# Optimization experiments

Measured on AMD Instinct MI355X. Metric: run time of the kernel, lower is better.

Reference implementation:

```python
import jax, jax.numpy as jnp
import numpy as np

EPS = 1e-12  # torch F.normalize eps

def _normalize(x, axis=-1):
    n = jnp.linalg.norm(x, axis=axis, keepdims=True)
    return x / jnp.maximum(n, EPS)

def setup_inputs() -> dict:
    key = jax.random.key(0)
    ks = jax.random.split(key, 6)
    B, D_in, T, Dc, K = 16, 1024, 4096, 8, 1024
    return {
        "z": jax.random.normal(ks[0], (B, D_in, T), jnp.float32),
        "in_w": jax.random.normal(ks[1], (Dc, D_in), jnp.float32) * 0.02,
        "in_b": jax.random.normal(ks[2], (Dc,), jnp.float32) * 0.02,
        "out_w": jax.random.normal(ks[3], (D_in, Dc), jnp.float32) * 0.02,
        "out_b": jax.random.normal(ks[4], (D_in,), jnp.float32) * 0.02,
        "codebook": jax.random.normal(ks[5], (K, Dc), jnp.float32),
    }

def reference(z, in_w, in_b, out_w, out_b, codebook):
    sg = jax.lax.stop_gradient
    # in_proj: kernel-size-1 conv == per-timestep linear. z: [B, D_in, T] -> z_e: [B, Dc, T]
    z_e = jnp.einsum('od,bdt->bot', in_w, z) + in_b[None, :, None]
    zt = jnp.swapaxes(z_e, 1, 2)  # [B, T, Dc]
    B, T, Dc = zt.shape
    # decode_latents: cosine-normalized squared-distance argmin over codebook
    en = _normalize(zt)                      # [B, T, Dc]
    cn = _normalize(codebook)                # [K, Dc]
    dist = (jnp.sum(en * en, -1, keepdims=True)
            - 2.0 * jnp.einsum('btd,kd->btk', en, cn)
            + jnp.sum(cn * cn, -1)[None, None, :])  # [B, T, K]
    indices = jnp.argmax(-dist, axis=-1)     # [B, T] int
    zq_td = codebook[indices]                # [B, T, Dc] (gather from unnormalized codebook)
    # losses (mean over channel+time dims per batch element)
    commitment_loss = jnp.mean((zt - sg(zq_td)) ** 2, axis=(1, 2))
    codebook_loss = jnp.mean((zq_td - sg(zt)) ** 2, axis=(1, 2))
    # rotation trick: R = I - 2 r r^T + 2 q e^T, applied fused (never materialize BxTxDxD)
    e_norm = _normalize(sg(zt))
    q_norm = _normalize(sg(zq_td))
    r = _normalize(e_norm + q_norm)
    scaling = (jnp.linalg.norm(sg(zq_td), axis=-1)
               / jnp.clip(jnp.linalg.norm(sg(zt), axis=-1), 1e-8))[..., None]
    Rz = zt - 2.0 * r * jnp.sum(r * zt, -1, keepdims=True) \
            + 2.0 * q_norm * jnp.sum(e_norm * zt, -1, keepdims=True)
    zq_rot = scaling * Rz                    # [B, T, Dc]
    zq = jnp.swapaxes(zq_rot, 1, 2)          # [B, Dc, T]
    # out_proj
    z_q_out = jnp.einsum('od,bdt->bot', out_w, zq) + out_b[None, :, None]  # [B, D_in, T]
    return (z_q_out, commitment_loss, codebook_loss, indices.astype(jnp.int32), z_e)
```

## Files before the change

kernel.cpp:

```cpp
#include <hip/hip_runtime.h>
#include <math.h>

#define NB   16
#define DIN  1024
#define TT   4096
#define DC   8
#define NK   1024
#define TA   128
#define NTA  (TT/TA)
#define NPG  16
#define KCP  (NK/NPG)

#define OFF_CL  ((size_t)NB*DIN*TT)
#define OFF_CB  (OFF_CL + NB)
#define OFF_IDX (OFF_CB + NB)
#define OFF_ZE  (OFF_IDX + (size_t)NB*TT)

__global__ __launch_bounds__(512, 4) void vq_mega(const float* __restrict__ z,
    const float* __restrict__ in_w, const float* __restrict__ in_b,
    const float* __restrict__ out_w, const float* __restrict__ out_b,
    const float* __restrict__ cbk, float* __restrict__ dout,
    float* __restrict__ lpart)
{
  __shared__ float regA[DIN*DC];
  __shared__ float regB[8*TA*DC];
  __shared__ float ze_s[DC*TA];
  float2* cand = (float2*)regB;
  float*  cn2  = regB + 4096;
  float*  obs  = regB + 5120;
  float*  zq_s = regB + 6144;
  float*  lred = regB + 7168;

  const int tid = threadIdx.x;
  const int tb = blockIdx.x, b = blockIdx.y;
  const int t0 = tb*TA;

  for (int i = tid; i < DIN*DC; i += 512) {
    const int d = i >> 3, o = i & 7;
    regA[i] = in_w[o*DIN + d];
  }
  __syncthreads();
  {
    const int sub = tid >> 6, l = tid & 63;
    const int dbase = sub*128;
    const float* zp = z + ((size_t)b*DIN + dbase)*TT + t0 + 2*l;
    float ax[DC], ay[DC];
    #pragma unroll
    for (int o = 0; o < DC; ++o) { ax[o] = 0.f; ay[o] = 0.f; }
    #pragma unroll 8
    for (int d = 0; d < 128; ++d) {
      const float2 v = *(const float2*)&zp[(size_t)d*TT];
      const float4 w0 = *(const float4*)&regA[(dbase+d)*DC];
      const float4 w1 = *(const float4*)&regA[(dbase+d)*DC+4];
      ax[0] = fmaf(v.x, w0.x, ax[0]);  ay[0] = fmaf(v.y, w0.x, ay[0]);
      ax[1] = fmaf(v.x, w0.y, ax[1]);  ay[1] = fmaf(v.y, w0.y, ay[1]);
      ax[2] = fmaf(v.x, w0.z, ax[2]);  ay[2] = fmaf(v.y, w0.z, ay[2]);
      ax[3] = fmaf(v.x, w0.w, ax[3]);  ay[3] = fmaf(v.y, w0.w, ay[3]);
      ax[4] = fmaf(v.x, w1.x, ax[4]);  ay[4] = fmaf(v.y, w1.x, ay[4]);
      ax[5] = fmaf(v.x, w1.y, ax[5]);  ay[5] = fmaf(v.y, w1.y, ay[5]);
      ax[6] = fmaf(v.x, w1.z, ax[6]);  ay[6] = fmaf(v.y, w1.z, ay[6]);
      ax[7] = fmaf(v.x, w1.w, ax[7]);  ay[7] = fmaf(v.y, w1.w, ay[7]);
    }
    float* pa = &regB[((size_t)sub*TA + 2*l)*DC];
    *(float4*)&pa[0]    = make_float4(ax[0], ax[1], ax[2], ax[3]);
    *(float4*)&pa[4]    = make_float4(ax[4], ax[5], ax[6], ax[7]);
    *(float4*)&pa[DC]   = make_float4(ay[0], ay[1], ay[2], ay[3]);
    *(float4*)&pa[DC+4] = make_float4(ay[4], ay[5], ay[6], ay[7]);
  }
  __syncthreads();
  {
    const int t = tid & 127, oq = tid >> 7;
    const int o0 = 2*oq;
    float2 p = *(const float2*)&regB[(0*TA + t)*DC + o0];
    float s0 = p.x, s1 = p.y;
    #pragma unroll
    for (int c = 1; c < 8; ++c) {
      p = *(const float2*)&regB[(c*TA + t)*DC + o0];
      s0 += p.x; s1 += p.y;
    }
    const float v0 = s0 + in_b[o0];
    const float v1 = s1 + in_b[o0+1];
    ze_s[o0*TA + t]     = v0;
    ze_s[(o0+1)*TA + t] = v1;
    dout[OFF_ZE + ((size_t)b*DC + o0)*TT + t0 + t]     = v0;
    dout[OFF_ZE + ((size_t)b*DC + o0+1)*TT + t0 + t]   = v1;
  }
  __syncthreads();

  for (int k = tid; k < NK; k += 512) {
    float c[DC];
    const float4 c0 = *(const float4*)&cbk[k*DC];
    const float4 c1 = *(const float4*)&cbk[k*DC+4];
    c[0]=c0.x; c[1]=c0.y; c[2]=c0.z; c[3]=c0.w;
    c[4]=c1.x; c[5]=c1.y; c[6]=c1.z; c[7]=c1.w;
    float ss = 0.f;
    #pragma unroll
    for (int i = 0; i < DC; ++i) ss = fmaf(c[i], c[i], ss);
    const float den = fmaxf(sqrtf(ss), 1e-12f);
    float s2 = 0.f;
    #pragma unroll
    for (int i = 0; i < DC; ++i) { const float v = c[i]/den; regA[k*DC+i] = v; s2 = fmaf(v, v, s2); }
    cn2[k] = s2;
  }
  __syncthreads();

  {
    const int pg = tid >> 5, l = tid & 31;
    const int k0 = pg*KCP;
    float en[4][DC], en2v[4];
    #pragma unroll
    for (int m = 0; m < 4; ++m) {
      const int t = l + 32*m;
      float e[DC];
      #pragma unroll
      for (int o = 0; o < DC; ++o) e[o] = ze_s[o*TA + t];
      float se = 0.f;
      #pragma unroll
      for (int i = 0; i < DC; ++i) se = fmaf(e[i], e[i], se);
      const float dene = fmaxf(sqrtf(se), 1e-12f);
      float s2 = 0.f;
      #pragma unroll
      for (int i = 0; i < DC; ++i) { en[m][i] = e[i]/dene; s2 = fmaf(en[m][i], en[m][i], s2); }
      en2v[m] = s2;
    }
    float bd[4]; int bk[4];
    #pragma unroll
    for (int m = 0; m < 4; ++m) { bd[m] = 3.4e38f; bk[m] = k0; }
    #pragma unroll 2
    for (int k = 0; k < KCP; ++k) {
      const float4 a0 = *(const float4*)&regA[(k0+k)*DC];
      const float4 a1 = *(const float4*)&regA[(k0+k)*DC+4];
      const float c2 = cn2[k0+k];
      #pragma unroll
      for (int m = 0; m < 4; ++m) {
        float dacc = en[m][0]*a0.x;
        dacc = fmaf(en[m][1], a0.y, dacc);
        dacc = fmaf(en[m][2], a0.z, dacc);
        dacc = fmaf(en[m][3], a0.w, dacc);
        dacc = fmaf(en[m][4], a1.x, dacc);
        dacc = fmaf(en[m][5], a1.y, dacc);
        dacc = fmaf(en[m][6], a1.z, dacc);
        dacc = fmaf(en[m][7], a1.w, dacc);
        const float dist = (en2v[m] - 2.0f*dacc) + c2;
        if (dist < bd[m]) { bd[m] = dist; bk[m] = k0 + k; }
      }
    }
    #pragma unroll
    for (int m = 0; m < 4; ++m)
      cand[pg*TA + l + 32*m] = make_float2(bd[m], __int_as_float(bk[m]));
  }
  __syncthreads();

  if (tid < TA) {
    float bdm = cand[tid].x;
    int bkm = __float_as_int(cand[tid].y);
    #pragma unroll
    for (int p = 1; p < NPG; ++p) {
      const float2 c = cand[p*TA + tid];
      if (c.x < bdm) { bdm = c.x; bkm = __float_as_int(c.y); }
    }
    dout[OFF_IDX + (size_t)b*TT + t0 + tid] = (float)bkm;

    float e[DC], en_[DC];
    #pragma unroll
    for (int o = 0; o < DC; ++o) e[o] = ze_s[o*TA + tid];
    float se = 0.f;
    #pragma unroll
    for (int i = 0; i < DC; ++i) se = fmaf(e[i], e[i], se);
    const float ne = sqrtf(se);
    const float dene = fmaxf(ne, 1e-12f);
    #pragma unroll
    for (int i = 0; i < DC; ++i) en_[i] = e[i]/dene;

    float q[DC];
    {
      const float4 q0 = *(const float4*)&cbk[bkm*DC];
      const float4 q1 = *(const float4*)&cbk[bkm*DC+4];
      q[0]=q0.x; q[1]=q0.y; q[2]=q0.z; q[3]=q0.w;
      q[4]=q1.x; q[5]=q1.y; q[6]=q1.z; q[7]=q1.w;
    }
    float cl = 0.f;
    #pragma unroll
    for (int i = 0; i < DC; ++i) { const float d = e[i]-q[i]; cl = fmaf(d, d, cl); }

    float sq = 0.f;
    #pragma unroll
    for (int i = 0; i < DC; ++i) sq = fmaf(q[i], q[i], sq);
    const float nq = sqrtf(sq);
    const float denq = fmaxf(nq, 1e-12f);
    float qn[DC], rr[DC];
    float sr = 0.f;
    #pragma unroll
    for (int i = 0; i < DC; ++i) { qn[i] = q[i]/denq; rr[i] = en_[i]+qn[i]; sr = fmaf(rr[i], rr[i], sr); }
    const float denr = fmaxf(sqrtf(sr), 1e-12f);
    float r_[DC];
    float rdz = 0.f, edz = 0.f;
    #pragma unroll
    for (int i = 0; i < DC; ++i) { r_[i] = rr[i]/denr; rdz = fmaf(r_[i], e[i], rdz); edz = fmaf(en_[i], e[i], edz); }
    const float scal = nq / fmaxf(ne, 1e-8f);
    #pragma unroll
    for (int i = 0; i < DC; ++i) {
      const float v = scal * ((e[i] - 2.0f*r_[i]*rdz) + 2.0f*qn[i]*edz);
      zq_s[i*TA + tid] = v;
    }
    lred[tid] = cl;
  } else {
    const int ti = tid - TA;
    for (int i = ti; i < DIN*DC; i += 512-TA) regA[i] = out_w[i];
    for (int i = ti; i < DIN; i += 512-TA) obs[i] = out_b[i];
  }
  __syncthreads();
  for (int s = TA/2; s > 0; s >>= 1) {
    if (tid < s) lred[tid] += lred[tid + s];
    __syncthreads();
  }
  if (tid == 0) lpart[b*NTA + tb] = lred[0];

  {
    const int sub3 = tid >> 6, tl2 = tid & 63;
    const int obase = sub3*128;
    const int tt2 = tl2*2;
    float zx[DC], zy[DC];
    #pragma unroll
    for (int c = 0; c < DC; ++c) {
      zx[c] = zq_s[c*TA + tt2];
      zy[c] = zq_s[c*TA + tt2 + 1];
    }
    float* op = dout + ((size_t)b*DIN + obase)*TT + t0 + tt2;
    #pragma unroll 4
    for (int o = 0; o < 128; ++o) {
      const float4 w0 = *(const float4*)&regA[(obase+o)*DC];
      const float4 w1 = *(const float4*)&regA[(obase+o)*DC+4];
      const float bv = obs[obase+o];
      float s0 = bv, s1 = bv;
      s0 = fmaf(zx[0], w0.x, s0);  s1 = fmaf(zy[0], w0.x, s1);
      s0 = fmaf(zx[1], w0.y, s0);  s1 = fmaf(zy[1], w0.y, s1);
      s0 = fmaf(zx[2], w0.z, s0);  s1 = fmaf(zy[2], w0.z, s1);
      s0 = fmaf(zx[3], w0.w, s0);  s1 = fmaf(zy[3], w0.w, s1);
      s0 = fmaf(zx[4], w1.x, s0);  s1 = fmaf(zy[4], w1.x, s1);
      s0 = fmaf(zx[5], w1.y, s0);  s1 = fmaf(zy[5], w1.y, s1);
      s0 = fmaf(zx[6], w1.z, s0);  s1 = fmaf(zy[6], w1.z, s1);
      s0 = fmaf(zx[7], w1.w, s0);  s1 = fmaf(zy[7], w1.w, s1);
      *(float2*)&op[(size_t)o*TT] = make_float2(s0, s1);
    }
  }
}

__global__ void vq_fin(const float* __restrict__ lpart, float* __restrict__ dout)
{
  const int b = threadIdx.x;
  if (b < NB) {
    float s = 0.f;
    for (int j = 0; j < NTA; ++j) s += lpart[b*NTA + j];
    const float v = s / (float)(TT*DC);
    dout[OFF_CL + b] = v;
    dout[OFF_CB + b] = v;
  }
}

extern "C" void kernel_launch(void* const* d_in, const int* in_sizes, int n_in,
                              void* d_out, int out_size, void* d_ws, size_t ws_size,
                              hipStream_t stream) {
  const float* z     = (const float*)d_in[0];
  const float* in_w  = (const float*)d_in[1];
  const float* in_b  = (const float*)d_in[2];
  const float* out_w = (const float*)d_in[3];
  const float* out_b = (const float*)d_in[4];
  const float* cbk   = (const float*)d_in[5];
  float* out = (float*)d_out;
  float* LP  = (float*)d_ws;

  vq_mega<<<dim3(NTA, NB), 512, 0, stream>>>(z, in_w, in_b, out_w, out_b, cbk, out, LP);
  vq_fin <<<1, 256, 0, stream>>>(LP, out);
}
```

Before: 137.1 us.

## Process two time tiles per block and stage all weights in LDS once

The kernel now launches half as many 1D blocks, and each block loops over two (batch, time-tile) pairs. The input weights, normalized codebook, output weights and bias each get their own shared buffers and are loaded once per block rather than once per tile. The aim is to cut the repeated global weight loads and codebook normalization. In exchange, shared memory grows to roughly 144KB per block, which likely limits each CU to one 512-thread block. That reduces latency hiding for a bandwidth-bound kernel, and launch bounds are relaxed to reflect it.

```diff
diff --git a/kernel.cpp b/kernel.cpp
--- a/kernel.cpp
+++ b/kernel.cpp
@@ -10,83 +10,37 @@
 #define NTA  (TT/TA)
 #define NPG  16
 #define KCP  (NK/NPG)
+#define ITERS 2
 
 #define OFF_CL  ((size_t)NB*DIN*TT)
 #define OFF_CB  (OFF_CL + NB)
 #define OFF_IDX (OFF_CB + NB)
 #define OFF_ZE  (OFF_IDX + (size_t)NB*TT)
 
-__global__ __launch_bounds__(512, 4) void vq_mega(const float* __restrict__ z,
+__global__ __launch_bounds__(512, 2) void vq_mega(const float* __restrict__ z,
     const float* __restrict__ in_w, const float* __restrict__ in_b,
     const float* __restrict__ out_w, const float* __restrict__ out_b,
     const float* __restrict__ cbk, float* __restrict__ dout,
     float* __restrict__ lpart)
 {
-  __shared__ float regA[DIN*DC];
-  __shared__ float regB[8*TA*DC];
+  __shared__ float wt[DIN*DC];
+  __shared__ float cn[NK*DC];
+  __shared__ float cn2[NK];
+  __shared__ float wo[DIN*DC];
+  __shared__ float obs[DIN];
+  __shared__ float pacc[8*TA*DC];
   __shared__ float ze_s[DC*TA];
-  float2* cand = (float2*)regB;
-  float*  cn2  = regB + 4096;
-  float*  obs  = regB + 5120;
-  float*  zq_s = regB + 6144;
-  float*  lred = regB + 7168;
+  __shared__ float zq_s[DC*TA];
+  __shared__ float lred[TA];
+  float2* cand = (float2*)pacc;
 
   const int tid = threadIdx.x;
-  const int tb = blockIdx.x, b = blockIdx.y;
-  const int t0 = tb*TA;
+  const int bid = blockIdx.x;
 
   for (int i = tid; i < DIN*DC; i += 512) {
     const int d = i >> 3, o = i & 7;
-    regA[i] = in_w[o*DIN + d];
-  }
-  __syncthreads();
-  {
-    const int sub = tid >> 6, l = tid & 63;
-    const int dbase = sub*128;
-    const float* zp = z + ((size_t)b*DIN + dbase)*TT + t0 + 2*l;
-    float ax[DC], ay[DC];
-    #pragma unroll
-    for (int o = 0; o < DC; ++o) { ax[o] = 0.f; ay[o] = 0.f; }
-    #pragma unroll 8
-    for (int d = 0; d < 128; ++d) {
-      const float2 v = *(const float2*)&zp[(size_t)d*TT];
-      const float4 w0 = *(const float4*)&regA[(dbase+d)*DC];
-      const float4 w1 = *(const float4*)&regA[(dbase+d)*DC+4];
-      ax[0] = fmaf(v.x, w0.x, ax[0]);  ay[0] = fmaf(v.y, w0.x, ay[0]);
-      ax[1] = fmaf(v.x, w0.y, ax[1]);  ay[1] = fmaf(v.y, w0.y, ay[1]);
-      ax[2] = fmaf(v.x, w0.z, ax[2]);  ay[2] = fmaf(v.y, w0.z, ay[2]);
-      ax[3] = fmaf(v.x, w0.w, ax[3]);  ay[3] = fmaf(v.y, w0.w, ay[3]);
-      ax[4] = fmaf(v.x, w1.x, ax[4]);  ay[4] = fmaf(v.y, w1.x, ay[4]);
-      ax[5] = fmaf(v.x, w1.y, ax[5]);  ay[5] = fmaf(v.y, w1.y, ay[5]);
-      ax[6] = fmaf(v.x, w1.z, ax[6]);  ay[6] = fmaf(v.y, w1.z, ay[6]);
-      ax[7] = fmaf(v.x, w1.w, ax[7]);  ay[7] = fmaf(v.y, w1.w, ay[7]);
-    }
-    float* pa = &regB[((size_t)sub*TA + 2*l)*DC];
-    *(float4*)&pa[0]    = make_float4(ax[0], ax[1], ax[2], ax[3]);
-    *(float4*)&pa[4]    = make_float4(ax[4], ax[5], ax[6], ax[7]);
-    *(float4*)&pa[DC]   = make_float4(ay[0], ay[1], ay[2], ay[3]);
-    *(float4*)&pa[DC+4] = make_float4(ay[4], ay[5], ay[6], ay[7]);
-  }
-  __syncthreads();
-  {
-    const int t = tid & 127, oq = tid >> 7;
-    const int o0 = 2*oq;
-    float2 p = *(const float2*)&regB[(0*TA + t)*DC + o0];
-    float s0 = p.x, s1 = p.y;
-    #pragma unroll
-    for (int c = 1; c < 8; ++c) {
-      p = *(const float2*)&regB[(c*TA + t)*DC + o0];
-      s0 += p.x; s1 += p.y;
-    }
-    const float v0 = s0 + in_b[o0];
-    const float v1 = s1 + in_b[o0+1];
-    ze_s[o0*TA + t]     = v0;
-    ze_s[(o0+1)*TA + t] = v1;
-    dout[OFF_ZE + ((size_t)b*DC + o0)*TT + t0 + t]     = v0;
-    dout[OFF_ZE + ((size_t)b*DC + o0+1)*TT + t0 + t]   = v1;
-  }
-  __syncthreads();
-
+    wt[i] = in_w[o*DIN + d];
+  }
   for (int k = tid; k < NK; k += 512) {
     float c[DC];
     const float4 c0 = *(const float4*)&cbk[k*DC];
@@ -99,149 +53,201 @@
     const float den = fmaxf(sqrtf(ss), 1e-12f);
     float s2 = 0.f;
     #pragma unroll
-    for (int i = 0; i < DC; ++i) { const float v = c[i]/den; regA[k*DC+i] = v; s2 = fmaf(v, v, s2); }
+    for (int i = 0; i < DC; ++i) { const float v = c[i]/den; cn[k*DC+i] = v; s2 = fmaf(v, v, s2); }
     cn2[k] = s2;
   }
+  for (int i = tid; i < DIN*DC; i += 512) wo[i] = out_w[i];
+  for (int i = tid; i < DIN; i += 512) obs[i] = out_b[i];
   __syncthreads();
 
-  {
-    const int pg = tid >> 5, l = tid & 31;
-    const int k0 = pg*KCP;
-    float en[4][DC], en2v[4];
-    #pragma unroll
-    for (int m = 0; m < 4; ++m) {
-      const int t = l + 32*m;
-      float e[DC];
-      #pragma unroll
-      for (int o = 0; o < DC; ++o) e[o] = ze_s[o*TA + t];
+  for (int it = 0; it < ITERS; ++it) {
+    const int tau = bid*ITERS + it;
+    const int b = tau >> 5, tb = tau & 31;
+    const int t0 = tb*TA;
+
+    {
+      const int sub = tid >> 6, l = tid & 63;
+      const int dbase = sub*128;
+      const float* zp = z + ((size_t)b*DIN + dbase)*TT + t0 + 2*l;
+      float ax[DC], ay[DC];
+      #pragma unroll
+      for (int o = 0; o < DC; ++o) { ax[o] = 0.f; ay[o] = 0.f; }
+      #pragma unroll 16
+      for (int d = 0; d < 128; ++d) {
+        const float2 v = *(const float2*)&zp[(size_t)d*TT];
+        const float4 w0 = *(const float4*)&wt[(dbase+d)*DC];
+        const float4 w1 = *(const float4*)&wt[(dbase+d)*DC+4];
+        ax[0] = fmaf(v.x, w0.x, ax[0]);  ay[0] = fmaf(v.y, w0.x, ay[0]);
+        ax[1] = fmaf(v.x, w0.y, ax[1]);  ay[1] = fmaf(v.y, w0.y, ay[1]);
+        ax[2] = fmaf(v.x, w0.z, ax[2]);  ay[2] = fmaf(v.y, w0.z, ay[2]);
+        ax[3] = fmaf(v.x, w0.w, ax[3]);  ay[3] = fmaf(v.y, w0.w, ay[3]);
+        ax[4] = fmaf(v.x, w1.x, ax[4]);  ay[4] = fmaf(v.y, w1.x, ay[4]);
+        ax[5] = fmaf(v.x, w1.y, ax[5]);  ay[5] = fmaf(v.y, w1.y, ay[5]);
+        ax[6] = fmaf(v.x, w1.z, ax[6]);  ay[6] = fmaf(v.y, w1.z, ay[6]);
+        ax[7] = fmaf(v.x, w1.w, ax[7]);  ay[7] = fmaf(v.y, w1.w, ay[7]);
+      }
+      float* pa = &pacc[((size_t)sub*TA + 2*l)*DC];
+      *(float4*)&pa[0]    = make_float4(ax[0], ax[1], ax[2], ax[3]);
+      *(float4*)&pa[4]    = make_float4(ax[4], ax[5], ax[6], ax[7]);
+      *(float4*)&pa[DC]   = make_float4(ay[0], ay[1], ay[2], ay[3]);
+      *(float4*)&pa[DC+4] = make_float4(ay[4], ay[5], ay[6], ay[7]);
+    }
+    __syncthreads();
+
+    {
+      const int t = tid & 127, oq = tid >> 7;
+      const int o0 = 2*oq;
+      float2 p = *(const float2*)&pacc[(0*TA + t)*DC + o0];
+      float s0 = p.x, s1 = p.y;
+      #pragma unroll
+      for (int c = 1; c < 8; ++c) {
+        p = *(const float2*)&pacc[(c*TA + t)*DC + o0];
+        s0 += p.x; s1 += p.y;
+      }
+      const float v0 = s0 + in_b[o0];
+      const float v1 = s1 + in_b[o0+1];
+      ze_s[o0*TA + t]     = v0;
+      ze_s[(o0+1)*TA + t] = v1;
+      dout[OFF_ZE + ((size_t)b*DC + o0)*TT + t0 + t]   = v0;
+      dout[OFF_ZE + ((size_t)b*DC + o0+1)*TT + t0 + t] = v1;
+    }
+    __syncthreads();
+
+    {
+      const int pg = tid >> 5, l = tid & 31;
+      const int k0 = pg*KCP;
+      float en[4][DC], en2v[4];
+      #pragma unroll
+      for (int m = 0; m < 4; ++m) {
+        const int t = l + 32*m;
+        float e[DC];
+        #pragma unroll
+        for (int o = 0; o < DC; ++o) e[o] = ze_s[o*TA + t];
+        float se = 0.f;
+        #pragma unroll
+        for (int i = 0; i < DC; ++i) se = fmaf(e[i], e[i], se);
+        const float dene = fmaxf(sqrtf(se), 1e-12f);
+        float s2 = 0.f;
+        #pragma unroll
+        for (int i = 0; i < DC; ++i) { en[m][i] = e[i]/dene; s2 = fmaf(en[m][i], en[m][i], s2); }
+        en2v[m] = s2;
+      }
+      float bd[4]; int bk[4];
+      #pragma unroll
+      for (int m = 0; m < 4; ++m) { bd[m] = 3.4e38f; bk[m] = k0; }
+      #pragma unroll 2
+      for (int k = 0; k < KCP; ++k) {
+        const float4 a0 = *(const float4*)&cn[(k0+k)*DC];
+        const float4 a1 = *(const float4*)&cn[(k0+k)*DC+4];
+        const float c2 = cn2[k0+k];
+        #pragma unroll
+        for (int m = 0; m < 4; ++m) {
+          float dacc = en[m][0]*a0.x;
+          dacc = fmaf(en[m][1], a0.y, dacc);
+          dacc = fmaf(en[m][2], a0.z, dacc);
+          dacc = fmaf(en[m][3], a0.w, dacc);
+          dacc = fmaf(en[m][4], a1.x, dacc);
+          dacc = fmaf(en[m][5], a1.y, dacc);
+          dacc = fmaf(en[m][6], a1.z, dacc);
+          dacc = fmaf(en[m][7], a1.w, dacc);
+          const float dist = (en2v[m] - 2.0f*dacc) + c2;
+          if (dist < bd[m]) { bd[m] = dist; bk[m] = k0 + k; }
+        }
+      }
+      #pragma unroll
+      for (int m = 0; m < 4; ++m)
+        cand[pg*TA + l + 32*m] = make_float2(bd[m], __int_as_float(bk[m]));
+    }
+    __syncthreads();
+
+    if (tid < TA) {
+      float bdm = cand[tid].x;
+      int bkm = __float_as_int(cand[tid].y);
+      #pragma unroll
+      for (int p = 1; p < NPG; ++p) {
+        const float2 c = cand[p*TA + tid];
+        if (c.x < bdm) { bdm = c.x; bkm = __float_as_int(c.y); }
+      }
+      dout[OFF_IDX + (size_t)b*TT + t0 + tid] = (float)bkm;
+
+      float e[DC], en_[DC];
+      #pragma unroll
+      for (int o = 0; o < DC; ++o) e[o] = ze_s[o*TA + tid];
       float se = 0.f;
       #pragma unroll
       for (int i = 0; i < DC; ++i) se = fmaf(e[i], e[i], se);
-      const float dene = fmaxf(sqrtf(se), 1e-12f);
-      float s2 = 0.f;
-      #pragma unroll
-      for (int i = 0; i < DC; ++i) { en[m][i] = e[i]/dene; s2 = fmaf(en[m][i], en[m][i], s2); }
-      en2v[m] = s2;
-    }
-    float bd[4]; int bk[4];
-    #pragma unroll
-    for (int m = 0; m < 4; ++m) { bd[m] = 3.4e38f; bk[m] = k0; }
-    #pragma unroll 2
-    for (int k = 0; k < KCP; ++k) {
-      const float4 a0 = *(const float4*)&regA[(k0+k)*DC];
-      const float4 a1 = *(const float4*)&regA[(k0+k)*DC+4];
-      const float c2 = cn2[k0+k];
-      #pragma unroll
-      for (int m = 0; m < 4; ++m) {
-        float dacc = en[m][0]*a0.x;
-        dacc = fmaf(en[m][1], a0.y, dacc);
-        dacc = fmaf(en[m][2], a0.z, dacc);
-        dacc = fmaf(en[m][3], a0.w, dacc);
-        dacc = fmaf(en[m][4], a1.x, dacc);
-        dacc = fmaf(en[m][5], a1.y, dacc);
-        dacc = fmaf(en[m][6], a1.z, dacc);
-        dacc = fmaf(en[m][7], a1.w, dacc);
-        const float dist = (en2v[m] - 2.0f*dacc) + c2;
-        if (dist < bd[m]) { bd[m] = dist; bk[m] = k0 + k; }
-      }
-    }
-    #pragma unroll
-    for (int m = 0; m < 4; ++m)
-      cand[pg*TA + l + 32*m] = make_float2(bd[m], __int_as_float(bk[m]));
-  }
-  __syncthreads();
-
-  if (tid < TA) {
-    float bdm = cand[tid].x;
-    int bkm = __float_as_int(cand[tid].y);
-    #pragma unroll
-    for (int p = 1; p < NPG; ++p) {
-      const float2 c = cand[p*TA + tid];
-      if (c.x < bdm) { bdm = c.x; bkm = __float_as_int(c.y); }
-    }
-    dout[OFF_IDX + (size_t)b*TT + t0 + tid] = (float)bkm;
-
-    float e[DC], en_[DC];
-    #pragma unroll
-    for (int o = 0; o < DC; ++o) e[o] = ze_s[o*TA + tid];
-    float se = 0.f;
-    #pragma unroll
-    for (int i = 0; i < DC; ++i) se = fmaf(e[i], e[i], se);
-    const float ne = sqrtf(se);
-    const float dene = fmaxf(ne, 1e-12f);
-    #pragma unroll
-    for (int i = 0; i < DC; ++i) en_[i] = e[i]/dene;
-
-    float q[DC];
-    {
-      const float4 q0 = *(const float4*)&cbk[bkm*DC];
-      const float4 q1 = *(const float4*)&cbk[bkm*DC+4];
-      q[0]=q0.x; q[1]=q0.y; q[2]=q0.z; q[3]=q0.w;
-      q[4]=q1.x; q[5]=q1.y; q[6]=q1.z; q[7]=q1.w;
-    }
-    float cl = 0.f;
-    #pragma unroll
-    for (int i = 0; i < DC; ++i) { const float d = e[i]-q[i]; cl = fmaf(d, d, cl); }
-
-    float sq = 0.f;
-    #pragma unroll
-    for (int i = 0; i < DC; ++i) sq = fmaf(q[i], q[i], sq);
-    const float nq = sqrtf(sq);
-    const float denq = fmaxf(nq, 1e-12f);
-    float qn[DC], rr[DC];
-    float sr = 0.f;
-    #pragma unroll
-    for (int i = 0; i < DC; ++i) { qn[i] = q[i]/denq; rr[i] = en_[i]+qn[i]; sr = fmaf(rr[i], rr[i], sr); }
-    const float denr = fmaxf(sqrtf(sr), 1e-12f);
-    float r_[DC];
-    float rdz = 0.f, edz = 0.f;
-    #pragma unroll
-    for (int i = 0; i < DC; ++i) { r_[i] = rr[i]/denr; rdz = fmaf(r_[i], e[i], rdz); edz = fmaf(en_[i], e[i], edz); }
-    const float scal = nq / fmaxf(ne, 1e-8f);
-    #pragma unroll
-    for (int i = 0; i < DC; ++i) {
-      const float v = scal * ((e[i] - 2.0f*r_[i]*rdz) + 2.0f*qn[i]*edz);
-      zq_s[i*TA + tid] = v;
-    }
-    lred[tid] = cl;
-  } else {
-    const int ti = tid - TA;
-    for (int i = ti; i < DIN*DC; i += 512-TA) regA[i] = out_w[i];
-    for (int i = ti; i < DIN; i += 512-TA) obs[i] = out_b[i];
-  }
-  __syncthreads();
-  for (int s = TA/2; s > 0; s >>= 1) {
-    if (tid < s) lred[tid] += lred[tid + s];
-    __syncthreads();
-  }
-  if (tid == 0) lpart[b*NTA + tb] = lred[0];
-
-  {
-    const int sub3 = tid >> 6, tl2 = tid & 63;
-    const int obase = sub3*128;
-    const int tt2 = tl2*2;
-    float zx[DC], zy[DC];
-    #pragma unroll
-    for (int c = 0; c < DC; ++c) {
-      zx[c] = zq_s[c*TA + tt2];
-      zy[c] = zq_s[c*TA + tt2 + 1];
-    }
-    float* op = dout + ((size_t)b*DIN + obase)*TT + t0 + tt2;
-    #pragma unroll 4
-    for (int o = 0; o < 128; ++o) {
-      const float4 w0 = *(const float4*)&regA[(obase+o)*DC];
-      const float4 w1 = *(const float4*)&regA[(obase+o)*DC+4];
-      const float bv = obs[obase+o];
-      float s0 = bv, s1 = bv;
-      s0 = fmaf(zx[0], w0.x, s0);  s1 = fmaf(zy[0], w0.x, s1);
-      s0 = fmaf(zx[1], w0.y, s0);  s1 = fmaf(zy[1], w0.y, s1);
-      s0 = fmaf(zx[2], w0.z, s0);  s1 = fmaf(zy[2], w0.z, s1);
-      s0 = fmaf(zx[3], w0.w, s0);  s1 = fmaf(zy[3], w0.w, s1);
-      s0 = fmaf(zx[4], w1.x, s0);  s1 = fmaf(zy[4], w1.x, s1);
-      s0 = fmaf(zx[5], w1.y, s0);  s1 = fmaf(zy[5], w1.y, s1);
-      s0 = fmaf(zx[6], w1.z, s0);  s1 = fmaf(zy[6], w1.z, s1);
-      s0 = fmaf(zx[7], w1.w, s0);  s1 = fmaf(zy[7], w1.w, s1);
-      *(float2*)&op[(size_t)o*TT] = make_float2(s0, s1);
+      const float ne = sqrtf(se);
+      const float dene = fmaxf(ne, 1e-12f);
+      #pragma unroll
+      for (int i = 0; i < DC; ++i) en_[i] = e[i]/dene;
+
+      float q[DC];
+      {
+        const float4 q0 = *(const float4*)&cbk[bkm*DC];
+        const float4 q1 = *(const float4*)&cbk[bkm*DC+4];
+        q[0]=q0.x; q[1]=q0.y; q[2]=q0.z; q[3]=q0.w;
+        q[4]=q1.x; q[5]=q1.y; q[6]=q1.z; q[7]=q1.w;
+      }
+      float cl = 0.f;
+      #pragma unroll
+      for (int i = 0; i < DC; ++i) { const float d = e[i]-q[i]; cl = fmaf(d, d, cl); }
+
+      float sq = 0.f;
+      #pragma unroll
+      for (int i = 0; i < DC; ++i) sq = fmaf(q[i], q[i], sq);
+      const float nq = sqrtf(sq);
+      const float denq = fmaxf(nq, 1e-12f);
+      float qn[DC], rr[DC];
+      float sr = 0.f;
+      #pragma unroll
+      for (int i = 0; i < DC; ++i) { qn[i] = q[i]/denq; rr[i] = en_[i]+qn[i]; sr = fmaf(rr[i], rr[i], sr); }
+      const float denr = fmaxf(sqrtf(sr), 1e-12f);
+      float r_[DC];
+      float rdz = 0.f, edz = 0.f;
+      #pragma unroll
+      for (int i = 0; i < DC; ++i) { r_[i] = rr[i]/denr; rdz = fmaf(r_[i], e[i], rdz); edz = fmaf(en_[i], e[i], edz); }
+      const float scal = nq / fmaxf(ne, 1e-8f);
+      #pragma unroll
+      for (int i = 0; i < DC; ++i) {
+        const float v = scal * ((e[i] - 2.0f*r_[i]*rdz) + 2.0f*qn[i]*edz);
+        zq_s[i*TA + tid] = v;
+      }
+      lred[tid] = cl;
+    }
+    __syncthreads();
+    for (int s = TA/2; s > 0; s >>= 1) {
+      if (tid < s) lred[tid] += lred[tid + s];
+      __syncthreads();
+    }
+    if (tid == 0) lpart[b*NTA + tb] = lred[0];
+
+    {
+      const int sub3 = tid >> 6, tl2 = tid & 63;
+      const int obase = sub3*128;
+      const int tt2 = tl2*2;
+      float zx[DC], zy[DC];
+      #pragma unroll
+      for (int c = 0; c < DC; ++c) {
+        zx[c] = zq_s[c*TA + tt2];
+        zy[c] = zq_s[c*TA + tt2 + 1];
+      }
+      float* op = dout + ((size_t)b*DIN + obase)*TT + t0 + tt2;
+      #pragma unroll 4
+      for (int o = 0; o < 128; ++o) {
+        const float4 w0 = *(const float4*)&wo[(obase+o)*DC];
+        const float4 w1 = *(const float4*)&wo[(obase+o)*DC+4];
+        const float bv = obs[obase+o];
+        float s0 = bv, s1 = bv;
+        s0 = fmaf(zx[0], w0.x, s0);  s1 = fmaf(zy[0], w0.x, s1);
+        s0 = fmaf(zx[1], w0.y, s0);  s1 = fmaf(zy[1], w0.y, s1);
+        s0 = fmaf(zx[2], w0.z, s0);  s1 = fmaf(zy[2], w0.z, s1);
+        s0 = fmaf(zx[3], w0.w, s0);  s1 = fmaf(zy[3], w0.w, s1);
+        s0 = fmaf(zx[4], w1.x, s0);  s1 = fmaf(zy[4], w1.x, s1);
+        s0 = fmaf(zx[5], w1.y, s0);  s1 = fmaf(zy[5], w1.y, s1);
+        s0 = fmaf(zx[6], w1.z, s0);  s1 = fmaf(zy[6], w1.z, s1);
+        s0 = fmaf(zx[7], w1.w, s0);  s1 = fmaf(zy[7], w1.w, s1);
+        *(float2*)&op[(size_t)o*TT] = make_float2(s0, s1);
+      }
     }
   }
 }
@@ -270,6 +276,6 @@
   float* out = (float*)d_out;
   float* LP  = (float*)d_ws;
 
-  vq_mega<<<dim3(NTA, NB), 512, 0, stream>>>(z, in_w, in_b, out_w, out_b, cbk, out, LP);
+  vq_mega<<<dim3(NB*NTA/ITERS), 512, 0, stream>>>(z, in_w, in_b, out_w, out_b, cbk, out, LP);
   vq_fin <<<1, 256, 0, stream>>>(LP, out);
 }
```

Result: slower. 144.1 us (+5.1%).
